# Optimization experiments

Measured on AMD Instinct MI355X. Metric: run time of the kernel, lower is better.

Reference implementation:

```python
import jax, jax.numpy as jnp
import numpy as np

N = 100000
E = 3200000
IN_C, H1, H2 = 512, 64, 32


def gcn_norm(edge_index, edge_weight, num_nodes):
    """PyG gcn_norm with add_self_loops=True: D^-1/2 (A+I) D^-1/2 edge weights."""
    row, col = edge_index[0], edge_index[1]
    loop = jnp.arange(num_nodes, dtype=edge_index.dtype)
    row = jnp.concatenate([row, loop])
    col = jnp.concatenate([col, loop])
    w = jnp.concatenate([edge_weight, jnp.ones((num_nodes,), edge_weight.dtype)])
    deg = jax.ops.segment_sum(w, col, num_segments=num_nodes)
    dinv = jnp.where(deg > 0, jax.lax.rsqrt(jnp.maximum(deg, 1e-12)), 0.0)
    wnorm = dinv[row] * w * dinv[col]
    return row, col, wnorm


def gcn_conv(x, W, b, row, col, wnorm, num_nodes):
    h = x @ W                                   # [N, out] linear first (out <= in)
    msg = wnorm[:, None] * h[row]               # gather + per-edge scale  [E+N, out]
    out = jax.ops.segment_sum(msg, col, num_segments=num_nodes)
    return out + b


def setup_inputs() -> dict:
    key = jax.random.key(0)
    ks = jax.random.split(key, 9)
    x = jax.random.normal(ks[0], (N, IN_C), dtype=jnp.float32)
    edge_index = jax.random.randint(ks[1], (2, E), 0, N, dtype=jnp.int64)
    edge_weight = jax.random.uniform(ks[2], (E,), dtype=jnp.float32)
    # Glorot-style init for GCN linear weights, zero bias (PyG defaults).
    def glorot(k, fan_in, fan_out):
        s = np.sqrt(6.0 / (fan_in + fan_out)).astype(np.float32)
        return jax.random.uniform(k, (fan_in, fan_out), jnp.float32, -s, s)
    return {
        "x": x,
        "edge_index": edge_index,
        "edge_weight": edge_weight,
        "W1": glorot(ks[3], IN_C, H1), "b1": jnp.zeros((H1,), jnp.float32),
        "W2": glorot(ks[4], H1, H2),  "b2": jnp.zeros((H2,), jnp.float32),
        "W3": glorot(ks[5], H2, 1),   "b3": jnp.zeros((1,), jnp.float32),
    }


def reference(x, edge_index, edge_weight, W1, b1, W2, b2, W3, b3):
    # Inference mode: dropout is identity (training=False).
    row, col, wnorm = gcn_norm(edge_index, edge_weight, N)  # cached=True: shared across layers
    h = jax.nn.relu(gcn_conv(x, W1, b1, row, col, wnorm, N))
    h = jax.nn.relu(gcn_conv(h, W2, b2, row, col, wnorm, N))
    h = gcn_conv(h, W3, b3, row, col, wnorm, N)
    return h.reshape(-1)  # [N]
```

## Files before the change

kernel.cpp:

```cpp
#include <hip/hip_runtime.h>

constexpr int BLK = 256;
constexpr int NBLKBIN = 512;
constexpr int MAXNB   = 1024;

typedef __bf16 bf16x8 __attribute__((ext_vector_type(8)));
typedef float  f32x4  __attribute__((ext_vector_type(4)));

__device__ __forceinline__ float blo(unsigned u) { return __uint_as_float(u << 16); }
__device__ __forceinline__ float bhi(unsigned u) { return __uint_as_float(u & 0xffff0000u); }

__global__ void k_detect(const int* __restrict__ ei, int e, int* __restrict__ flag) {
    if (blockIdx.x == 0 && threadIdx.x == 0) {
        int is64 = 1;
        for (int i = 0; i < 16; ++i)
            if (ei[2 * i + 1] != 0) { is64 = 0; break; }
        *flag = is64;
    }
}

__device__ __forceinline__ int load_idx(const void* ei, size_t pos, int is64) {
    if (is64) return (int)((const long long*)ei)[pos];
    return ((const int*)ei)[pos];
}

__global__ void k_zero_i(int* __restrict__ p, int n) {
    long i = (long)blockIdx.x * BLK + threadIdx.x;
    if (i < n) p[i] = 0;
}

__global__ __launch_bounds__(256) void k_binhist(const void* __restrict__ ei, int e,
                                                 const int* __restrict__ flag,
                                                 int* __restrict__ bucket_cnt, int nb) {
    __shared__ int hist[MAXNB];
    const int t = threadIdx.x;
    for (int b = t; b < nb; b += 256) hist[b] = 0;
    __syncthreads();
    const int is64 = *flag;
    const int chunk = (e + NBLKBIN - 1) / NBLKBIN;
    const int i0 = blockIdx.x * chunk;
    const int i1 = min(e, i0 + chunk);
    for (int i = i0 + t; i < i1; i += 256) {
        int dst = load_idx(ei, (size_t)e + i, is64);
        atomicAdd(&hist[dst >> 7], 1);
    }
    __syncthreads();
    for (int b = t; b < nb; b += 256) {
        int c = hist[b];
        if (c) atomicAdd(&bucket_cnt[b], c);
    }
}

__global__ void k_scanbkt(const int* __restrict__ cnt, int* __restrict__ offs,
                          int* __restrict__ cursor, int nb, int e) {
    __shared__ int sh[256];
    const int t = threadIdx.x;
    const int base = t * 4;
    int v[4]; int s = 0;
#pragma unroll
    for (int k = 0; k < 4; ++k) {
        int i = base + k;
        v[k] = (i < nb) ? cnt[i] : 0;
        s += v[k];
    }
    sh[t] = s;
    __syncthreads();
    for (int d = 1; d < 256; d <<= 1) {
        int x = (t >= d) ? sh[t - d] : 0;
        __syncthreads();
        sh[t] += x;
        __syncthreads();
    }
    int excl = (t == 0) ? 0 : sh[t - 1];
#pragma unroll
    for (int k = 0; k < 4; ++k) {
        int i = base + k;
        if (i < nb) { offs[i] = excl; cursor[i] = excl; excl += v[k]; }
    }
    if (t == 255) offs[nb] = e;
}

__global__ __launch_bounds__(256) void k_binscatter(const void* __restrict__ ei,
                                                    const float* __restrict__ ew, int e,
                                                    const int* __restrict__ flag,
                                                    int* __restrict__ bucket_cursor,
                                                    int2* __restrict__ binned, int nb) {
    __shared__ int hist[MAXNB];
    const int t = threadIdx.x;
    for (int b = t; b < nb; b += 256) hist[b] = 0;
    __syncthreads();
    const int is64 = *flag;
    const int chunk = (e + NBLKBIN - 1) / NBLKBIN;
    const int i0 = blockIdx.x * chunk;
    const int i1 = min(e, i0 + chunk);
    for (int i = i0 + t; i < i1; i += 256) {
        int dst = load_idx(ei, (size_t)e + i, is64);
        atomicAdd(&hist[dst >> 7], 1);
    }
    __syncthreads();
    for (int b = t; b < nb; b += 256) {
        int c = hist[b];
        int base = 0;
        if (c) base = atomicAdd(&bucket_cursor[b], c);
        hist[b] = base;
    }
    __syncthreads();
    for (int i = i0 + t; i < i1; i += 256) {
        int dst = load_idx(ei, (size_t)e + i, is64);
        int src = load_idx(ei, (size_t)i, is64);
        float w = ew[i];
        int bin = dst >> 7;
        int pos = atomicAdd(&hist[bin], 1);
        binned[pos] = make_int2(src | ((dst & 127) << 20), __float_as_int(w));
    }
}

__global__ __launch_bounds__(256) void k_bucketcnt(const int* __restrict__ bucket_offs,
                                                   const int2* __restrict__ binned,
                                                   int* __restrict__ counts,
                                                   float* __restrict__ dinv, int n) {
    __shared__ int   icnt[128];
    __shared__ float facc[128];
    const int t = threadIdx.x;
    const int k = blockIdx.x;
    if (t < 128) { icnt[t] = 0; facc[t] = 0.f; }
    __syncthreads();
    const int j0 = bucket_offs[k], j1 = bucket_offs[k + 1];
    for (int j = j0 + t; j < j1; j += 256) {
        int2 p = binned[j];
        int dl = ((unsigned)p.x) >> 20;
        atomicAdd(&icnt[dl], 1);
        atomicAdd(&facc[dl], __int_as_float(p.y));
    }
    __syncthreads();
    if (t < 128) {
        int nd = k * 128 + t;
        if (nd < n) {
            counts[nd] = icnt[t];
            dinv[nd] = rsqrtf(1.0f + facc[t]);
        }
    }
}

__global__ void k_scan1(const int* __restrict__ in, int* __restrict__ out,
                        int* __restrict__ bsum, int n) {
    __shared__ int sh[256];
    const int t = threadIdx.x;
    const int base = blockIdx.x * 1024 + t * 4;
    int v[4];
    int s = 0;
#pragma unroll
    for (int k = 0; k < 4; ++k) {
        int i = base + k;
        v[k] = (i < n) ? in[i] : 0;
        s += v[k];
    }
    sh[t] = s;
    __syncthreads();
    for (int d = 1; d < 256; d <<= 1) {
        int x = (t >= d) ? sh[t - d] : 0;
        __syncthreads();
        sh[t] += x;
        __syncthreads();
    }
    int excl = (t == 0) ? 0 : sh[t - 1];
    if (t == 255) bsum[blockIdx.x] = sh[255];
#pragma unroll
    for (int k = 0; k < 4; ++k) {
        int i = base + k;
        if (i < n) { out[i] = excl; excl += v[k]; }
    }
}

__global__ void k_scan2(int* __restrict__ bsum, int nb) {
    __shared__ int sh[128];
    const int t = threadIdx.x;
    sh[t] = (t < nb) ? bsum[t] : 0;
    __syncthreads();
    for (int d = 1; d < 128; d <<= 1) {
        int x = (t >= d) ? sh[t - d] : 0;
        __syncthreads();
        sh[t] += x;
        __syncthreads();
    }
    if (t < nb) bsum[t] = (t == 0) ? 0 : sh[t - 1];
}

__global__ void k_scan3(int* __restrict__ offs, const int* __restrict__ scanned,
                        const int* __restrict__ bsum, int n, int e) {
    long i = (long)blockIdx.x * BLK + threadIdx.x;
    if (i < n) offs[i] = scanned[i] + bsum[i >> 10];
    if (i == 0) offs[n] = e;
}

__global__ __launch_bounds__(256) void k_place(const int* __restrict__ bucket_offs,
                                               const int2* __restrict__ binned,
                                               const int* __restrict__ offs,
                                               const float* __restrict__ dinv,
                                               int2* __restrict__ csrp, int n) {
    __shared__ int cur[128];
    const int t = threadIdx.x;
    const int k = blockIdx.x;
    if (t < 128) {
        int nd = k * 128 + t;
        cur[t] = (nd < n) ? offs[nd] : 0;
    }
    __syncthreads();
    const int j0 = bucket_offs[k], j1 = bucket_offs[k + 1];
    for (int j = j0 + t; j < j1; j += 256) {
        int2 p = binned[j];
        int dl  = ((unsigned)p.x) >> 20;
        int src = p.x & 0xFFFFF;
        int pos = atomicAdd(&cur[dl], 1);
        float w2 = __int_as_float(p.y) * dinv[src];
        csrp[pos] = make_int2(src, __float_as_int(w2));
    }
}

__global__ void k_wcvt_frag(const float* __restrict__ W, __bf16* __restrict__ Wtf) {
    int i = blockIdx.x * BLK + threadIdx.x;
    if (i >= 4096) return;
    int lane = i & 63;
    int t    = (i >> 6) & 3;
    int k0c  = i >> 8;
    int col  = t * 16 + (lane & 15);
    int kbase = k0c * 32 + (lane >> 4) * 8;
    bf16x8 v;
#pragma unroll
    for (int j = 0; j < 8; ++j) v[j] = (__bf16)W[(size_t)(kbase + j) * 64 + col];
    *(bf16x8*)(Wtf + (size_t)i * 8) = v;
}

__global__ void k_wcvt_frag2(const float* __restrict__ W, __bf16* __restrict__ Wtf2) {
    int i = threadIdx.x;
    int lane = i & 63;
    int ct   = i >> 6;
    int t = ct & 1, chunk = ct >> 1;
    int col  = t * 16 + (lane & 15);
    int kbase = chunk * 32 + (lane >> 4) * 8;
    bf16x8 v;
#pragma unroll
    for (int j = 0; j < 8; ++j) v[j] = (__bf16)W[(size_t)(kbase + j) * 32 + col];
    *(bf16x8*)(Wtf2 + (size_t)i * 8) = v;
}

__global__ __launch_bounds__(256) void k_gemm1_mfma(const float* __restrict__ X,
                                                    const __bf16* __restrict__ Wtf,
                                                    __bf16* __restrict__ H, int nrows) {
    const int wave = threadIdx.x >> 6;
    const int lane = threadIdx.x & 63;
    const int l15  = lane & 15;
    const int lq   = lane >> 4;
    const long rbase = (long)blockIdx.x * 64 + wave * 16;

    long arow = rbase + l15;
    if (arow >= nrows) arow = nrows - 1;
    const float4* xr4 = (const float4*)(X + (size_t)arow * 512) + lq * 2;

    f32x4 acc[4] = {{0.f,0.f,0.f,0.f},{0.f,0.f,0.f,0.f},{0.f,0.f,0.f,0.f},{0.f,0.f,0.f,0.f}};

    float4 pa[4][2];
#pragma unroll
    for (int p = 0; p < 4; ++p) { pa[p][0] = xr4[p * 8]; pa[p][1] = xr4[p * 8 + 1]; }

#pragma unroll
    for (int k0c = 0; k0c < 16; ++k0c) {
        const int s = k0c & 3;
        float4 a0 = pa[s][0];
        float4 a1 = pa[s][1];
        if (k0c + 4 < 16) {
            pa[s][0] = xr4[(k0c + 4) * 8];
            pa[s][1] = xr4[(k0c + 4) * 8 + 1];
        }
        bf16x8 af;
        af[0] = (__bf16)a0.x; af[1] = (__bf16)a0.y; af[2] = (__bf16)a0.z; af[3] = (__bf16)a0.w;
        af[4] = (__bf16)a1.x; af[5] = (__bf16)a1.y; af[6] = (__bf16)a1.z; af[7] = (__bf16)a1.w;
#pragma unroll
        for (int t = 0; t < 4; ++t) {
            bf16x8 bf_ = *(const bf16x8*)(Wtf + ((size_t)(k0c * 4 + t) * 64 + lane) * 8);
            acc[t] = __builtin_amdgcn_mfma_f32_16x16x32_bf16(af, bf_, acc[t], 0, 0, 0);
        }
    }
#pragma unroll
    for (int t = 0; t < 4; ++t) {
#pragma unroll
        for (int r = 0; r < 4; ++r) {
            long row = rbase + lq * 4 + r;
            if (row < nrows) H[(size_t)row * 64 + t * 16 + l15] = (__bf16)acc[t][r];
        }
    }
}

__global__ __launch_bounds__(256) void k_gemm2_mfma(const __bf16* __restrict__ A,
                                                    const __bf16* __restrict__ Wtf2,
                                                    __bf16* __restrict__ H, int nrows) {
    const int wave = threadIdx.x >> 6;
    const int lane = threadIdx.x & 63;
    const int l15  = lane & 15;
    const int lq   = lane >> 4;
    const long rbase = (long)blockIdx.x * 64 + wave * 16;

    long arow = rbase + l15;
    if (arow >= nrows) arow = nrows - 1;

    f32x4 acc[2] = {{0.f,0.f,0.f,0.f},{0.f,0.f,0.f,0.f}};
#pragma unroll
    for (int c = 0; c < 2; ++c) {
        bf16x8 af = *(const bf16x8*)(A + (size_t)arow * 64 + c * 32 + lq * 8);
#pragma unroll
        for (int t = 0; t < 2; ++t) {
            bf16x8 bf_ = *(const bf16x8*)(Wtf2 + ((size_t)(c * 2 + t) * 64 + lane) * 8);
            acc[t] = __builtin_amdgcn_mfma_f32_16x16x32_bf16(af, bf_, acc[t], 0, 0, 0);
        }
    }
#pragma unroll
    for (int t = 0; t < 2; ++t) {
#pragma unroll
        for (int r = 0; r < 4; ++r) {
            long row = rbase + lq * 4 + r;
            if (row < nrows) H[(size_t)row * 32 + t * 16 + l15] = (__bf16)acc[t][r];
        }
    }
}

template <int K, bool RELU, bool OBF16>
__global__ __launch_bounds__(256) void k_prop_bf(const int* __restrict__ offs,
                                                 const int2* __restrict__ csrp,
                                                 const __bf16* __restrict__ hb,
                                                 const float* __restrict__ dinv,
                                                 const float* __restrict__ bias,
                                                 void* __restrict__ outv, int n) {
    constexpr int SUB = K / 2;
    constexpr int NPW = 64 / SUB;
    constexpr int NPB = 4 * NPW;
    const int t    = threadIdx.x;
    const int lane = t & 63;
    const int wave = t >> 6;
    const int chp  = lane & (SUB - 1);
    const int sub  = lane / SUB;
    const long nd  = (long)blockIdx.x * NPB + wave * NPW + sub;
    if (nd >= n) return;

    const unsigned short* h = (const unsigned short*)hb;
    const int j0 = offs[nd], j1 = offs[nd + 1];
    float a0 = 0.f, a1 = 0.f;
    int j = j0;
    for (; j + 3 < j1; j += 4) {
        int2 p0 = csrp[j];
        int2 p1 = csrp[j + 1];
        int2 p2 = csrp[j + 2];
        int2 p3 = csrp[j + 3];
        unsigned u0 = *(const unsigned*)(h + (size_t)p0.x * K + 2 * chp);
        unsigned u1 = *(const unsigned*)(h + (size_t)p1.x * K + 2 * chp);
        unsigned u2 = *(const unsigned*)(h + (size_t)p2.x * K + 2 * chp);
        unsigned u3 = *(const unsigned*)(h + (size_t)p3.x * K + 2 * chp);
        float w0 = __int_as_float(p0.y), w1 = __int_as_float(p1.y);
        float w2 = __int_as_float(p2.y), w3 = __int_as_float(p3.y);
        a0 = fmaf(w0, blo(u0), a0); a1 = fmaf(w0, bhi(u0), a1);
        a0 = fmaf(w1, blo(u1), a0); a1 = fmaf(w1, bhi(u1), a1);
        a0 = fmaf(w2, blo(u2), a0); a1 = fmaf(w2, bhi(u2), a1);
        a0 = fmaf(w3, blo(u3), a0); a1 = fmaf(w3, bhi(u3), a1);
    }
    for (; j < j1; ++j) {
        int2 p0 = csrp[j];
        unsigned u0 = *(const unsigned*)(h + (size_t)p0.x * K + 2 * chp);
        float w0 = __int_as_float(p0.y);
        a0 = fmaf(w0, blo(u0), a0);
        a1 = fmaf(w0, bhi(u0), a1);
    }
    const float di = dinv[nd];
    const float s  = di * di;
    unsigned us = *(const unsigned*)(h + (size_t)nd * K + 2 * chp);
    float2 bv = *(const float2*)(bias + 2 * chp);
    float o0 = fmaf(di, a0, fmaf(s, blo(us), bv.x));
    float o1 = fmaf(di, a1, fmaf(s, bhi(us), bv.y));
    if (RELU) { o0 = fmaxf(o0, 0.f); o1 = fmaxf(o1, 0.f); }
    if (OBF16) {
        unsigned short s0 = __builtin_bit_cast(unsigned short, (__bf16)o0);
        unsigned short s1 = __builtin_bit_cast(unsigned short, (__bf16)o1);
        ((unsigned*)outv)[(size_t)nd * (K / 2) + chp] = (unsigned)s0 | ((unsigned)s1 << 16);
    } else {
        *(float2*)((float*)outv + (size_t)nd * K + 2 * chp) = make_float2(o0, o1);
    }
}

__global__ void k_lin3(const float* __restrict__ X, const float* __restrict__ W3,
                       float* __restrict__ h3, int n) {
    long i = (long)blockIdx.x * BLK + threadIdx.x;
    if (i >= n) return;
    const float4* xr = (const float4*)(X + (size_t)i * 32);
    float acc = 0.f;
#pragma unroll
    for (int c = 0; c < 8; ++c) {
        float4 xv = xr[c];
        float4 wv = ((const float4*)W3)[c];
        acc = fmaf(xv.x, wv.x, acc);
        acc = fmaf(xv.y, wv.y, acc);
        acc = fmaf(xv.z, wv.z, acc);
        acc = fmaf(xv.w, wv.w, acc);
    }
    h3[i] = acc;
}

__global__ __launch_bounds__(256) void k_prop1(const int* __restrict__ offs,
                                               const int2* __restrict__ csrp,
                                               const float* __restrict__ h,
                                               const float* __restrict__ dinv,
                                               const float* __restrict__ bias,
                                               float* __restrict__ out, int n) {
    long nd = (long)blockIdx.x * BLK + threadIdx.x;
    if (nd >= n) return;
    const int j0 = offs[nd], j1 = offs[nd + 1];
    float acc = 0.f;
    int j = j0;
    for (; j + 3 < j1; j += 4) {
        int2 p0 = csrp[j];
        int2 p1 = csrp[j + 1];
        int2 p2 = csrp[j + 2];
        int2 p3 = csrp[j + 3];
        acc = fmaf(__int_as_float(p0.y), h[p0.x], acc);
        acc = fmaf(__int_as_float(p1.y), h[p1.x], acc);
        acc = fmaf(__int_as_float(p2.y), h[p2.x], acc);
        acc = fmaf(__int_as_float(p3.y), h[p3.x], acc);
    }
    for (; j < j1; ++j) {
        int2 p0 = csrp[j];
        acc = fmaf(__int_as_float(p0.y), h[p0.x], acc);
    }
    const float di = dinv[nd];
    out[nd] = fmaf(di, acc, fmaf(di * di, h[nd], bias[0]));
}

extern "C" void kernel_launch(void* const* d_in, const int* in_sizes, int n_in,
                              void* d_out, int out_size, void* d_ws, size_t ws_size,
                              hipStream_t stream) {
    const float* x  = (const float*)d_in[0];
    const void*  ei = d_in[1];
    const float* ew = (const float*)d_in[2];
    const float* W1 = (const float*)d_in[3];
    const float* b1 = (const float*)d_in[4];
    const float* W2 = (const float*)d_in[5];
    const float* b2 = (const float*)d_in[6];
    const float* W3 = (const float*)d_in[7];
    const float* b3 = (const float*)d_in[8];
    float* out = (float*)d_out;

    const int n = in_sizes[0] / 512;
    const int e = in_sizes[2];
    const int nb = (n + 127) >> 7;

    char* ws = (char*)d_ws;
    size_t off = 0;
    auto alloc = [&](size_t bytes) {
        void* p = ws + off;
        off = (off + bytes + 255) & ~(size_t)255;
        return p;
    };
    int*    flag     = (int*)   alloc(4);
    int2*   binned   = (int2*)  alloc((size_t)e * 8);
    __bf16* hbuf1    = (__bf16*)binned;
    int*    bkt_cnt  = (int*)   alloc((size_t)(MAXNB + 1) * 4);
    int*    bkt_offs = (int*)   alloc((size_t)(MAXNB + 1) * 4);
    int*    bkt_cur  = (int*)   alloc((size_t)(MAXNB + 1) * 4);
    int*    counts   = (int*)   alloc((size_t)n * 4);
    int*    offs     = (int*)   alloc((size_t)(n + 1) * 4);
    int*    bsum     = (int*)   alloc(512);
    int2*   csrp     = (int2*)  alloc((size_t)e * 8);
    float*  dinv     = (float*) alloc((size_t)n * 4);
    __bf16* pb64     = (__bf16*)alloc((size_t)n * 64 * 2);
    __bf16* hbuf2    = (__bf16*)alloc((size_t)n * 32 * 2);
    float*  pf32     = (float*) alloc((size_t)n * 32 * 4);
    float*  h3       = (float*) alloc((size_t)n * 4);
    __bf16* Wtf      = (__bf16*)alloc((size_t)512 * 64 * 2);
    __bf16* Wtf2     = (__bf16*)alloc((size_t)64 * 32 * 2);
    (void)ws_size; (void)n_in; (void)out_size;

    const int gb_n = (n + BLK - 1) / BLK;
    const int nb_scan = (n + 1023) / 1024;

    k_detect<<<1, 64, 0, stream>>>((const int*)ei, e, flag);

    k_zero_i<<<(nb + BLK - 1) / BLK, BLK, 0, stream>>>(bkt_cnt, nb);
    k_binhist<<<NBLKBIN, 256, 0, stream>>>(ei, e, flag, bkt_cnt, nb);
    k_scanbkt<<<1, 256, 0, stream>>>(bkt_cnt, bkt_offs, bkt_cur, nb, e);
    k_binscatter<<<NBLKBIN, 256, 0, stream>>>(ei, ew, e, flag, bkt_cur, binned, nb);
    k_bucketcnt<<<nb, 256, 0, stream>>>(bkt_offs, binned, counts, dinv, n);
    k_scan1<<<nb_scan, 256, 0, stream>>>(counts, counts, bsum, n);
    k_scan2<<<1, 128, 0, stream>>>(bsum, nb_scan);
    k_scan3<<<gb_n, BLK, 0, stream>>>(offs, counts, bsum, n, e);
    k_place<<<nb, 256, 0, stream>>>(bkt_offs, binned, offs, dinv, csrp, n);

    k_wcvt_frag<<<(4096 + BLK - 1) / BLK, BLK, 0, stream>>>(W1, Wtf);
    k_wcvt_frag2<<<1, 256, 0, stream>>>(W2, Wtf2);

    k_gemm1_mfma<<<(n + 63) / 64, 256, 0, stream>>>(x, Wtf, hbuf1, n);
    k_prop_bf<64, true, true><<<(n + 7) / 8, 256, 0, stream>>>(offs, csrp, hbuf1, dinv, b1, pb64, n);

    k_gemm2_mfma<<<(n + 63) / 64, 256, 0, stream>>>(pb64, Wtf2, hbuf2, n);
    k_prop_bf<32, true, false><<<(n + 15) / 16, 256, 0, stream>>>(offs, csrp, hbuf2, dinv, b2, pf32, n);

    k_lin3<<<gb_n, BLK, 0, stream>>>(pf32, W3, h3, n);
    k_prop1<<<gb_n, BLK, 0, stream>>>(offs, csrp, h3, dinv, b3, out, n);
}
```

Before: 390.8 us.

## Fuse layer-3 linear into layer-2 propagation and double GEMM1 rows per wave

Layer-2 propagation now applies the W3 dot product in its epilogue through a sub-wave shuffle reduction and writes h3 directly. This removes the k_lin3 launch and the round trip of the N×32 fp32 intermediate through memory. Separately, GEMM1 has each wave compute 32 rows instead of 16, so every W fragment load feeds two MFMAs, at the cost of more registers and a shallower X prefetch (2 stages instead of 4).

Result: no change. 384.6 us (-1.6%).

```diff
diff --git a/kernel.cpp b/kernel.cpp
--- a/kernel.cpp
+++ b/kernel.cpp
@@ -251,43 +251,55 @@
     const int lane = threadIdx.x & 63;
     const int l15  = lane & 15;
     const int lq   = lane >> 4;
-    const long rbase = (long)blockIdx.x * 64 + wave * 16;
-
-    long arow = rbase + l15;
-    if (arow >= nrows) arow = nrows - 1;
-    const float4* xr4 = (const float4*)(X + (size_t)arow * 512) + lq * 2;
-
-    f32x4 acc[4] = {{0.f,0.f,0.f,0.f},{0.f,0.f,0.f,0.f},{0.f,0.f,0.f,0.f},{0.f,0.f,0.f,0.f}};
-
-    float4 pa[4][2];
-#pragma unroll
-    for (int p = 0; p < 4; ++p) { pa[p][0] = xr4[p * 8]; pa[p][1] = xr4[p * 8 + 1]; }
+    const long rbase = (long)blockIdx.x * 128 + wave * 32;
+
+    long ar0 = rbase + l15;      if (ar0 >= nrows) ar0 = nrows - 1;
+    long ar1 = rbase + 16 + l15; if (ar1 >= nrows) ar1 = nrows - 1;
+    const float4* x0 = (const float4*)(X + (size_t)ar0 * 512) + lq * 2;
+    const float4* x1 = (const float4*)(X + (size_t)ar1 * 512) + lq * 2;
+
+    f32x4 acc[2][4];
+#pragma unroll
+    for (int r = 0; r < 2; ++r)
+#pragma unroll
+        for (int t = 0; t < 4; ++t) acc[r][t] = f32x4{0.f, 0.f, 0.f, 0.f};
+
+    float4 pa[2][2][2];
+#pragma unroll
+    for (int s = 0; s < 2; ++s) {
+        pa[s][0][0] = x0[s * 8]; pa[s][0][1] = x0[s * 8 + 1];
+        pa[s][1][0] = x1[s * 8]; pa[s][1][1] = x1[s * 8 + 1];
+    }
 
 #pragma unroll
     for (int k0c = 0; k0c < 16; ++k0c) {
-        const int s = k0c & 3;
-        float4 a0 = pa[s][0];
-        float4 a1 = pa[s][1];
-        if (k0c + 4 < 16) {
-            pa[s][0] = xr4[(k0c + 4) * 8];
-            pa[s][1] = xr4[(k0c + 4) * 8 + 1];
+        const int s = k0c & 1;
+        float4 a00 = pa[s][0][0], a01 = pa[s][0][1];
+        float4 a10 = pa[s][1][0], a11 = pa[s][1][1];
+        if (k0c + 2 < 16) {
+            pa[s][0][0] = x0[(k0c + 2) * 8]; pa[s][0][1] = x0[(k0c + 2) * 8 + 1];
+            pa[s][1][0] = x1[(k0c + 2) * 8]; pa[s][1][1] = x1[(k0c + 2) * 8 + 1];
         }
-        bf16x8 af;
-        af[0] = (__bf16)a0.x; af[1] = (__bf16)a0.y; af[2] = (__bf16)a0.z; af[3] = (__bf16)a0.w;
-        af[4] = (__bf16)a1.x; af[5] = (__bf16)a1.y; af[6] = (__bf16)a1.z; af[7] = (__bf16)a1.w;
+        bf16x8 af0, af1;
+        af0[0] = (__bf16)a00.x; af0[1] = (__bf16)a00.y; af0[2] = (__bf16)a00.z; af0[3] = (__bf16)a00.w;
+        af0[4] = (__bf16)a01.x; af0[5] = (__bf16)a01.y; af0[6] = (__bf16)a01.z; af0[7] = (__bf16)a01.w;
+        af1[0] = (__bf16)a10.x; af1[1] = (__bf16)a10.y; af1[2] = (__bf16)a10.z; af1[3] = (__bf16)a10.w;
+        af1[4] = (__bf16)a11.x; af1[5] = (__bf16)a11.y; af1[6] = (__bf16)a11.z; af1[7] = (__bf16)a11.w;
 #pragma unroll
         for (int t = 0; t < 4; ++t) {
             bf16x8 bf_ = *(const bf16x8*)(Wtf + ((size_t)(k0c * 4 + t) * 64 + lane) * 8);
-            acc[t] = __builtin_amdgcn_mfma_f32_16x16x32_bf16(af, bf_, acc[t], 0, 0, 0);
+            acc[0][t] = __builtin_amdgcn_mfma_f32_16x16x32_bf16(af0, bf_, acc[0][t], 0, 0, 0);
+            acc[1][t] = __builtin_amdgcn_mfma_f32_16x16x32_bf16(af1, bf_, acc[1][t], 0, 0, 0);
         }
     }
 #pragma unroll
-    for (int t = 0; t < 4; ++t) {
-#pragma unroll
-        for (int r = 0; r < 4; ++r) {
-            long row = rbase + lq * 4 + r;
-            if (row < nrows) H[(size_t)row * 64 + t * 16 + l15] = (__bf16)acc[t][r];
-        }
+    for (int rr = 0; rr < 2; ++rr)
+#pragma unroll
+    for (int t = 0; t < 4; ++t)
+#pragma unroll
+    for (int r = 0; r < 4; ++r) {
+        long row = rbase + rr * 16 + lq * 4 + r;
+        if (row < nrows) H[(size_t)row * 64 + t * 16 + l15] = (__bf16)acc[rr][t][r];
     }
 }
 
@@ -314,21 +326,21 @@
         }
     }
 #pragma unroll
-    for (int t = 0; t < 2; ++t) {
-#pragma unroll
-        for (int r = 0; r < 4; ++r) {
-            long row = rbase + lq * 4 + r;
-            if (row < nrows) H[(size_t)row * 32 + t * 16 + l15] = (__bf16)acc[t][r];
-        }
-    }
-}
-
-template <int K, bool RELU, bool OBF16>
+    for (int t = 0; t < 2; ++t)
+#pragma unroll
+    for (int r = 0; r < 4; ++r) {
+        long row = rbase + lq * 4 + r;
+        if (row < nrows) H[(size_t)row * 32 + t * 16 + l15] = (__bf16)acc[t][r];
+    }
+}
+
+template <int K, int EPI>
 __global__ __launch_bounds__(256) void k_prop_bf(const int* __restrict__ offs,
                                                  const int2* __restrict__ csrp,
                                                  const __bf16* __restrict__ hb,
                                                  const float* __restrict__ dinv,
                                                  const float* __restrict__ bias,
+                                                 const float* __restrict__ W3,
                                                  void* __restrict__ outv, int n) {
     constexpr int SUB = K / 2;
     constexpr int NPW = 64 / SUB;
@@ -374,32 +386,18 @@
     float2 bv = *(const float2*)(bias + 2 * chp);
     float o0 = fmaf(di, a0, fmaf(s, blo(us), bv.x));
     float o1 = fmaf(di, a1, fmaf(s, bhi(us), bv.y));
-    if (RELU) { o0 = fmaxf(o0, 0.f); o1 = fmaxf(o1, 0.f); }
-    if (OBF16) {
+    o0 = fmaxf(o0, 0.f); o1 = fmaxf(o1, 0.f);
+    if (EPI == 0) {
         unsigned short s0 = __builtin_bit_cast(unsigned short, (__bf16)o0);
         unsigned short s1 = __builtin_bit_cast(unsigned short, (__bf16)o1);
-        ((unsigned*)outv)[(size_t)nd * (K / 2) + chp] = (unsigned)s0 | ((unsigned)s1 << 16);
+        ((unsigned*)outv)[(size_t)nd * SUB + chp] = (unsigned)s0 | ((unsigned)s1 << 16);
     } else {
-        *(float2*)((float*)outv + (size_t)nd * K + 2 * chp) = make_float2(o0, o1);
-    }
-}
-
-__global__ void k_lin3(const float* __restrict__ X, const float* __restrict__ W3,
-                       float* __restrict__ h3, int n) {
-    long i = (long)blockIdx.x * BLK + threadIdx.x;
-    if (i >= n) return;
-    const float4* xr = (const float4*)(X + (size_t)i * 32);
-    float acc = 0.f;
-#pragma unroll
-    for (int c = 0; c < 8; ++c) {
-        float4 xv = xr[c];
-        float4 wv = ((const float4*)W3)[c];
-        acc = fmaf(xv.x, wv.x, acc);
-        acc = fmaf(xv.y, wv.y, acc);
-        acc = fmaf(xv.z, wv.z, acc);
-        acc = fmaf(xv.w, wv.w, acc);
-    }
-    h3[i] = acc;
+        float2 wv = *(const float2*)(W3 + 2 * chp);
+        float part = o0 * wv.x + o1 * wv.y;
+#pragma unroll
+        for (int d = SUB / 2; d >= 1; d >>= 1) part += __shfl_xor(part, d, SUB);
+        if (chp == 0) ((float*)outv)[nd] = part;
+    }
 }
 
 __global__ __launch_bounds__(256) void k_prop1(const int* __restrict__ offs,
@@ -469,7 +467,6 @@
     float*  dinv     = (float*) alloc((size_t)n * 4);
     __bf16* pb64     = (__bf16*)alloc((size_t)n * 64 * 2);
     __bf16* hbuf2    = (__bf16*)alloc((size_t)n * 32 * 2);
-    float*  pf32     = (float*) alloc((size_t)n * 32 * 4);
     float*  h3       = (float*) alloc((size_t)n * 4);
     __bf16* Wtf      = (__bf16*)alloc((size_t)512 * 64 * 2);
     __bf16* Wtf2     = (__bf16*)alloc((size_t)64 * 32 * 2);
@@ -493,12 +490,11 @@
     k_wcvt_frag<<<(4096 + BLK - 1) / BLK, BLK, 0, stream>>>(W1, Wtf);
     k_wcvt_frag2<<<1, 256, 0, stream>>>(W2, Wtf2);
 
-    k_gemm1_mfma<<<(n + 63) / 64, 256, 0, stream>>>(x, Wtf, hbuf1, n);
-    k_prop_bf<64, true, true><<<(n + 7) / 8, 256, 0, stream>>>(offs, csrp, hbuf1, dinv, b1, pb64, n);
+    k_gemm1_mfma<<<(n + 127) / 128, 256, 0, stream>>>(x, Wtf, hbuf1, n);
+    k_prop_bf<64, 0><<<(n + 7) / 8, 256, 0, stream>>>(offs, csrp, hbuf1, dinv, b1, nullptr, pb64, n);
 
     k_gemm2_mfma<<<(n + 63) / 64, 256, 0, stream>>>(pb64, Wtf2, hbuf2, n);
-    k_prop_bf<32, true, false><<<(n + 15) / 16, 256, 0, stream>>>(offs, csrp, hbuf2, dinv, b2, pf32, n);
-
-    k_lin3<<<gb_n, BLK, 0, stream>>>(pf32, W3, h3, n);
+    k_prop_bf<32, 1><<<(n + 15) / 16, 256, 0, stream>>>(offs, csrp, hbuf2, dinv, b2, W3, h3, n);
+
     k_prop1<<<gb_n, BLK, 0, stream>>>(offs, csrp, h3, dinv, b3, out, n);
 }
```
